# Kernel optimization log

Hardware: AMD Instinct MI355X
Metric: run time of the kernel (lower is better)

The kernel has to match this reference:

```python
import jax, jax.numpy as jnp
import numpy as np

B, P, Q, D_IN, H, DR = 16, 4096, 512, 512, 256, 256


def setup_inputs() -> dict:
    key = jax.random.key(0)
    ks = jax.random.split(key, 6)
    passage = jax.random.normal(ks[0], (B, P, D_IN), dtype=jnp.float32)
    question = jax.random.normal(ks[1], (B, Q, D_IN), dtype=jnp.float32)
    rep = jax.random.normal(ks[2], (B, Q, DR), dtype=jnp.float32)
    rep_p = jax.random.normal(ks[3], (B, P, DR), dtype=jnp.float32)
    p_mask = jnp.zeros((B, P), dtype=bool)  # True = padding position
    q_mask = jnp.zeros((B, Q), dtype=bool)
    # xavier-uniform-like init for U weight, stored as [in, out]
    limit = float(np.sqrt(6.0 / (D_IN + H)))
    W = jax.random.uniform(ks[4], (D_IN, H), dtype=jnp.float32, minval=-limit, maxval=limit)
    D = jnp.ones((1, H), dtype=jnp.float32)
    return {"passage": passage, "p_mask": p_mask, "question": question,
            "q_mask": q_mask, "rep": rep, "rep_p": rep_p, "W": W, "D": D,
            "is_training": 0}


def reference(passage, p_mask, question, q_mask, rep, rep_p, W, D, is_training):
    # inference path (is_training falsy): no dropout
    Up = jax.nn.relu(passage @ W)              # [B, P, H]
    Uq = jax.nn.relu(question @ W) * D         # [B, Q, H], scaled by diagonal D
    scores = jnp.einsum('bph,bqh->bpq', Up, Uq)  # [B, P, Q]
    # question -> passage direction (rep_p is not None)
    scores_T = jnp.where(p_mask[:, None, :], -jnp.inf, scores.transpose(0, 2, 1))  # [B, Q, P]
    alpha_p = jax.nn.softmax(scores_T, axis=-1)
    output_q = jnp.einsum('bqp,bpd->bqd', alpha_p, rep_p)  # [B, Q, DR]
    # passage -> question direction
    scores_m = jnp.where(q_mask[:, None, :], -jnp.inf, scores)  # [B, P, Q]
    alpha = jax.nn.softmax(scores_m, axis=-1)
    output = jnp.einsum('bpq,bqd->bpd', alpha, rep)  # [B, P, DR]
    return (output, output_q)
```

## Files before the change

### kernel.cpp

```cpp
#include <hip/hip_runtime.h>


typedef float  f32x4   __attribute__((ext_vector_type(4)));
typedef float  float4v __attribute__((ext_vector_type(4)));
typedef short  short8v __attribute__((ext_vector_type(8)));
typedef unsigned short us4 __attribute__((ext_vector_type(4)));
typedef unsigned short us8v __attribute__((ext_vector_type(8)));

#define MFMA16(a,b,c) __builtin_amdgcn_mfma_f32_16x16x32_bf16((a),(b),(c),0,0,0)

__device__ __forceinline__ unsigned short f2bf(float f) {
  unsigned int u = __builtin_bit_cast(unsigned int, f);
  u += 0x7FFFu + ((u >> 16) & 1u);
  return (unsigned short)(u >> 16);
}
__device__ __forceinline__ float bf2f(unsigned short h) {
  unsigned int u = (unsigned int)h << 16;
  return __builtin_bit_cast(float, u);
}
__device__ __forceinline__ void split2(float v, unsigned short& h, unsigned short& l) {
  h = f2bf(v);
  l = f2bf(v - bf2f(h));
}
__device__ __forceinline__ unsigned short enc16(float a, float cm) {
  float x = (a - cm + 20.f) * 3276.8f + 0.5f;
  x = fminf(fmaxf(x, 0.f), 65535.f);
  return (unsigned short)x;
}

__global__ __launch_bounds__(256) void transpose_all(
    const float* __restrict__ W, const float* __restrict__ rep,
    const float* __restrict__ rep_p,
    unsigned short* __restrict__ Wth, unsigned short* __restrict__ Wtl,
    unsigned short* __restrict__ repT, unsigned short* __restrict__ repTp)
{
  __shared__ float lTf[64][65];
  const int blk = blockIdx.x;
  const float* src; unsigned short* dst; unsigned short* dstl = nullptr;
  int srows; size_t r0, c0;
  if (blk < 4096) {
    int b = blk >> 8, tb = blk & 255;
    src = rep_p + (size_t)b * 4096 * 256;
    dst = repTp + (size_t)b * 256 * 4096;
    srows = 4096; r0 = (size_t)(tb >> 2) * 64; c0 = (size_t)(tb & 3) * 64;
  } else if (blk < 4608) {
    int rel = blk - 4096; int b = rel >> 5, tb = rel & 31;
    src = rep + (size_t)b * 512 * 256;
    dst = repT + (size_t)b * 256 * 512;
    srows = 512; r0 = (size_t)(tb >> 2) * 64; c0 = (size_t)(tb & 3) * 64;
  } else {
    int rel = blk - 4608;
    src = W; dst = Wth; dstl = Wtl;
    srows = 512; r0 = (size_t)(rel >> 2) * 64; c0 = (size_t)(rel & 3) * 64;
  }
  const int t = threadIdx.x;
#pragma unroll
  for (int j = 0; j < 4; ++j) {
    int idx = j * 256 + t;
    int r = idx >> 4, c4 = (idx & 15) * 4;
    float4v v = *(const float4v*)&src[(r0 + (size_t)r) * 256 + c0 + c4];
    lTf[r][c4 + 0] = v[0]; lTf[r][c4 + 1] = v[1];
    lTf[r][c4 + 2] = v[2]; lTf[r][c4 + 3] = v[3];
  }
  __syncthreads();
#pragma unroll
  for (int j = 0; j < 4; ++j) {
    int idx = j * 256 + t;
    int dr = idx >> 4, p4 = (idx & 15) * 4;
    size_t o = (c0 + (size_t)dr) * (size_t)srows + r0 + p4;
    if (!dstl) {
      us4 oh;
#pragma unroll
      for (int e = 0; e < 4; ++e) oh[e] = f2bf(lTf[p4 + e][dr]);
      *(us4*)&dst[o] = oh;
    } else {
      us4 oh, ol;
#pragma unroll
      for (int e = 0; e < 4; ++e) {
        unsigned short h, l; split2(lTf[p4 + e][dr], h, l);
        oh[e] = h; ol[e] = l;
      }
      *(us4*)&dst[o] = oh;
      *(us4*)&dstl[o] = ol;
    }
  }
}

template<int APPLY_D>
__global__ __launch_bounds__(256) void ugemm_kernel(
    const float* __restrict__ X,
    const unsigned short* __restrict__ Wth, const unsigned short* __restrict__ Wtl,
    const float* __restrict__ Dv,
    unsigned short* __restrict__ Uh, unsigned short* __restrict__ Ul)
{
  __shared__ unsigned short lAh[64 * 40], lAl[64 * 40];
  __shared__ unsigned short lBh[256 * 40], lBl[256 * 40];
  const int t = threadIdx.x;
  const int w = t >> 6, l = t & 63;
  const int l15 = l & 15, lg = l >> 4, kr = lg * 8;
  const size_t m0 = (size_t)blockIdx.x * 64;
  const int arow = t >> 2, ac = (t & 3) * 8;
  const float* asrc = X + (m0 + arow) * 512 + ac;

  f32x4 acc[4][4] = {};
  float4v va0, va1;
  short8v vbh[4], vbl[4];

  va0 = *(const float4v*)(asrc);
  va1 = *(const float4v*)(asrc + 4);
#pragma unroll
  for (int j = 0; j < 4; ++j) {
    int idx = j * 256 + t;
    int row = idx >> 2, c = (idx & 3) * 8;
    size_t g = (size_t)row * 512 + c;
    vbh[j] = *(const short8v*)&Wth[g];
    vbl[j] = *(const short8v*)&Wtl[g];
  }

  for (int k0 = 0; k0 < 512; k0 += 32) {
    short8v ph, pl;
#pragma unroll
    for (int e = 0; e < 4; ++e) {
      unsigned short h, lo;
      split2(va0[e], h, lo); ph[e] = (short)h; pl[e] = (short)lo;
      split2(va1[e], h, lo); ph[4 + e] = (short)h; pl[4 + e] = (short)lo;
    }
    __syncthreads();
    *(short8v*)&lAh[arow * 40 + ac] = ph;
    *(short8v*)&lAl[arow * 40 + ac] = pl;
#pragma unroll
    for (int j = 0; j < 4; ++j) {
      int idx = j * 256 + t;
      int row = idx >> 2, c = (idx & 3) * 8;
      *(short8v*)&lBh[row * 40 + c] = vbh[j];
      *(short8v*)&lBl[row * 40 + c] = vbl[j];
    }
    __syncthreads();
    if (k0 < 480) {
      va0 = *(const float4v*)(asrc + k0 + 32);
      va1 = *(const float4v*)(asrc + k0 + 36);
#pragma unroll
      for (int j = 0; j < 4; ++j) {
        int idx = j * 256 + t;
        int row = idx >> 2, c = (idx & 3) * 8;
        size_t g = (size_t)row * 512 + k0 + 32 + c;
        vbh[j] = *(const short8v*)&Wth[g];
        vbl[j] = *(const short8v*)&Wtl[g];
      }
    }
    short8v ah[4], al[4];
#pragma unroll
    for (int mi = 0; mi < 4; ++mi) {
      ah[mi] = *(const short8v*)&lAh[(mi * 16 + l15) * 40 + kr];
      al[mi] = *(const short8v*)&lAl[(mi * 16 + l15) * 40 + kr];
    }
#pragma unroll
    for (int ni = 0; ni < 4; ++ni) {
      int rr = (w * 64 + ni * 16 + l15) * 40 + kr;
      short8v bh = *(const short8v*)&lBh[rr];
      short8v bl = *(const short8v*)&lBl[rr];
#pragma unroll
      for (int mi = 0; mi < 4; ++mi) {
        acc[mi][ni] = MFMA16(ah[mi], bh, acc[mi][ni]);
        acc[mi][ni] = MFMA16(ah[mi], bl, acc[mi][ni]);
        acc[mi][ni] = MFMA16(al[mi], bh, acc[mi][ni]);
      }
    }
  }
#pragma unroll
  for (int mi = 0; mi < 4; ++mi)
#pragma unroll
    for (int ni = 0; ni < 4; ++ni)
#pragma unroll
      for (int r = 0; r < 4; ++r) {
        size_t row = m0 + mi * 16 + lg * 4 + r;
        int col = w * 64 + ni * 16 + l15;
        float v = acc[mi][ni][r];
        v = v > 0.f ? v : 0.f;
        if (APPLY_D) v *= Dv[col];
        unsigned short h, lo; split2(v, h, lo);
        Uh[row * 256 + col] = h;
        Ul[row * 256 + col] = lo;
      }
}

template<int STORE_S>
__global__ __launch_bounds__(512, 4) void dir2_kernel(
    const unsigned short* __restrict__ Uph, const unsigned short* __restrict__ Upl,
    const unsigned short* __restrict__ Uqh, const unsigned short* __restrict__ Uql,
    const unsigned short* __restrict__ repT, const unsigned char* __restrict__ qmask,
    const unsigned char* __restrict__ pmask, unsigned short* __restrict__ St,
    float* __restrict__ colmaxP, float* __restrict__ out)
{
  __shared__ __align__(16) unsigned char smem[68608];
  unsigned short* probs = (unsigned short*)smem;
  float* smax = (float*)(smem + 66560);
  float* ssum = (float*)(smem + 67584);

  const int id = blockIdx.x;
  const int b  = (id & 7) | ((id >> 9) << 3);
  const int p0 = ((id >> 3) & 63) * 64;
  const int t = threadIdx.x;
  const int w = t >> 6, l = t & 63;
  const int wr = w >> 2, wc = w & 3;
  const int l15 = l & 15, lg = l >> 4, kr = lg * 8;
  const int srow = t >> 2, sc = (t & 3) * 8;

  const unsigned short* UqBh = Uqh + (size_t)b * 512 * 256;
  const unsigned short* UqBl = Uql + (size_t)b * 512 * 256;
  const size_t aoff = ((size_t)b * 4096 + p0 + wr * 32 + l15) * 256 + kr;
  const unsigned short* pAh0 = Uph + aoff;
  const unsigned short* pAh1 = pAh0 + 16 * 256;
  const unsigned short* pAl0 = Upl + aoff;
  const unsigned short* pAl1 = pAl0 + 16 * 256;

  auto lbh = [&](int buf) { return (unsigned short*)(smem + buf * 20480); };
  auto lbl = [&](int buf) { return (unsigned short*)(smem + buf * 20480 + 10240); };

  f32x4 acc[2][8] = {};
  short8v cah0, cah1, cal0, cal1;
  short8v nah0, nah1, nal0, nal1;
  short8v rh, rl;

  cah0 = *(const short8v*)&pAh0[0];
  cah1 = *(const short8v*)&pAh1[0];
  cal0 = *(const short8v*)&pAl0[0];
  cal1 = *(const short8v*)&pAl1[0];
  {
    size_t g = (size_t)srow * 256 + sc;
    rh = *(const short8v*)&UqBh[g];
    rl = *(const short8v*)&UqBl[g];
  }
  *(short8v*)&lbh(0)[srow * 40 + sc] = rh;
  *(short8v*)&lbl(0)[srow * 40 + sc] = rl;
  __syncthreads();

  for (int k0 = 0; k0 < 8; ++k0) {
#pragma unroll
    for (int qh = 0; qh < 4; ++qh) {
      const int cur = qh & 1;
      const bool last = (k0 == 7) && (qh == 3);
      if (!last) {
        int nk0 = (qh == 3) ? k0 + 1 : k0;
        int nqh = (qh == 3) ? 0 : qh + 1;
        size_t g = (size_t)(nqh * 128 + srow) * 256 + nk0 * 32 + sc;
        rh = *(const short8v*)&UqBh[g];
        rl = *(const short8v*)&UqBl[g];
      }
      if (qh == 3 && k0 < 7) {
        size_t ao = (size_t)(k0 + 1) * 32;
        nah0 = *(const short8v*)&pAh0[ao];
        nah1 = *(const short8v*)&pAh1[ao];
        nal0 = *(const short8v*)&pAl0[ao];
        nal1 = *(const short8v*)&pAl1[ao];
      }
      const unsigned short* bhp = lbh(cur);
      const unsigned short* blp = lbl(cur);
#pragma unroll
      for (int qi = 0; qi < 2; ++qi) {
        int rr = (wc * 32 + qi * 16 + l15) * 40 + kr;
        short8v bh = *(const short8v*)&bhp[rr];
        short8v bl = *(const short8v*)&blp[rr];
        int j = qh * 2 + qi;
        acc[0][j] = MFMA16(cah0, bh, acc[0][j]);
        acc[0][j] = MFMA16(cah0, bl, acc[0][j]);
        acc[0][j] = MFMA16(cal0, bh, acc[0][j]);
        acc[1][j] = MFMA16(cah1, bh, acc[1][j]);
        acc[1][j] = MFMA16(cah1, bl, acc[1][j]);
        acc[1][j] = MFMA16(cal1, bh, acc[1][j]);
      }
      if (!last) {
        *(short8v*)&lbh(cur ^ 1)[srow * 40 + sc] = rh;
        *(short8v*)&lbl(cur ^ 1)[srow * 40 + sc] = rl;
      }
      if (qh == 3 && k0 < 7) { cah0 = nah0; cah1 = nah1; cal0 = nal0; cal1 = nal1; }
      __syncthreads();
    }
  }
  if (STORE_S) {
    const unsigned char* pmk = pmask + (size_t)b * 4096 + p0 + wr * 32;
    unsigned int pmw0 = *(const unsigned int*)&pmk[lg * 4];
    unsigned int pmw1 = *(const unsigned int*)&pmk[16 + lg * 4];
#pragma unroll
    for (int j = 0; j < 8; ++j) {
      int qcol = ((j >> 1) << 7) + wc * 32 + ((j & 1) << 4) + l15;
      float a0[4], a1[4];
      float cm = -1e30f;
#pragma unroll
      for (int r = 0; r < 4; ++r) {
        a0[r] = ((pmw0 >> (8 * r)) & 0xFFu) ? -1e30f : acc[0][j][r];
        a1[r] = ((pmw1 >> (8 * r)) & 0xFFu) ? -1e30f : acc[1][j][r];
        cm = fmaxf(cm, fmaxf(a0[r], a1[r]));
      }
      cm = fmaxf(cm, __shfl_xor(cm, 16));
      cm = fmaxf(cm, __shfl_xor(cm, 32));
      us4 e0, e1;
#pragma unroll
      for (int r = 0; r < 4; ++r) {
        e0[r] = enc16(a0[r], cm);
        e1[r] = enc16(a1[r], cm);
      }
      size_t sb = ((size_t)b * 512 + qcol) * 4096 + p0 + wr * 32 + lg * 4;
      *(us4*)&St[sb]      = e0;
      *(us4*)&St[sb + 16] = e1;
      if (l < 16)
        colmaxP[((size_t)b * 128 + (p0 >> 5) + wr) * 512 + qcol] = cm;
    }
  }
  const unsigned char* qm = qmask + (size_t)b * 512;
#pragma unroll
  for (int j = 0; j < 8; ++j) {
    int qcol = ((j >> 1) << 7) + wc * 32 + ((j & 1) << 4) + l15;
    if (qm[qcol]) {
#pragma unroll
      for (int mi = 0; mi < 2; ++mi)
#pragma unroll
        for (int r = 0; r < 4; ++r) acc[mi][j][r] = -1e30f;
    }
  }
#pragma unroll
  for (int mi = 0; mi < 2; ++mi)
#pragma unroll
    for (int r = 0; r < 4; ++r) {
      float v = acc[mi][0][r];
#pragma unroll
      for (int j = 1; j < 8; ++j) v = fmaxf(v, acc[mi][j][r]);
      v = fmaxf(v, __shfl_xor(v, 1)); v = fmaxf(v, __shfl_xor(v, 2));
      v = fmaxf(v, __shfl_xor(v, 4)); v = fmaxf(v, __shfl_xor(v, 8));
      if (l15 == 0) smax[wc * 64 + wr * 32 + mi * 16 + lg * 4 + r] = v;
    }
  __syncthreads();
  float Mx[2][4];
#pragma unroll
  for (int mi = 0; mi < 2; ++mi)
#pragma unroll
    for (int r = 0; r < 4; ++r) {
      int row = wr * 32 + mi * 16 + lg * 4 + r;
      Mx[mi][r] = fmaxf(fmaxf(smax[row], smax[64 + row]),
                        fmaxf(smax[128 + row], smax[192 + row]));
    }
  float rs[2][4] = {};
#pragma unroll
  for (int mi = 0; mi < 2; ++mi)
#pragma unroll
    for (int j = 0; j < 8; ++j)
#pragma unroll
      for (int r = 0; r < 4; ++r) {
        float ev = __expf(acc[mi][j][r] - Mx[mi][r]);
        acc[mi][j][r] = ev;
        rs[mi][r] += ev;
      }
#pragma unroll
  for (int mi = 0; mi < 2; ++mi)
#pragma unroll
    for (int r = 0; r < 4; ++r) {
      float v = rs[mi][r];
      v += __shfl_xor(v, 1); v += __shfl_xor(v, 2);
      v += __shfl_xor(v, 4); v += __shfl_xor(v, 8);
      if (l15 == 0) ssum[wc * 64 + wr * 32 + mi * 16 + lg * 4 + r] = v;
    }
#pragma unroll
  for (int mi = 0; mi < 2; ++mi)
#pragma unroll
    for (int j = 0; j < 8; ++j) {
      int qcol = ((j >> 1) << 7) + wc * 32 + ((j & 1) << 4) + l15;
#pragma unroll
      for (int r = 0; r < 4; ++r)
        probs[(wr * 32 + mi * 16 + lg * 4 + r) * 520 + qcol] = f2bf(acc[mi][j][r]);
    }
  __syncthreads();
  const unsigned short* rT = repT + (size_t)b * 131072;
  float invv[4][4];
#pragma unroll
  for (int mi = 0; mi < 4; ++mi)
#pragma unroll
    for (int r = 0; r < 4; ++r) {
      int row = mi * 16 + lg * 4 + r;
      invv[mi][r] = 1.0f / (ssum[row] + ssum[64 + row] +
                            ssum[128 + row] + ssum[192 + row]);
    }
  f32x4 acc2[4][2] = {};
  const unsigned short* rTb = rT + (size_t)(w * 32 + l15) * 512 + kr;
  short8v cb0 = *(const short8v*)(rTb);
  short8v cb1 = *(const short8v*)(rTb + 16 * 512);
  for (int k0 = 0; k0 < 512; k0 += 32) {
    int kn = (k0 + 32) & 511;
    short8v nb0 = *(const short8v*)(rTb + kn);
    short8v nb1 = *(const short8v*)(rTb + 16 * 512 + kn);
    short8v a0 = *(const short8v*)&probs[(l15) * 520 + k0 + kr];
    short8v a1 = *(const short8v*)&probs[(16 + l15) * 520 + k0 + kr];
    short8v a2 = *(const short8v*)&probs[(32 + l15) * 520 + k0 + kr];
    short8v a3 = *(const short8v*)&probs[(48 + l15) * 520 + k0 + kr];
    acc2[0][0] = MFMA16(a0, cb0, acc2[0][0]);
    acc2[1][0] = MFMA16(a1, cb0, acc2[1][0]);
    acc2[2][0] = MFMA16(a2, cb0, acc2[2][0]);
    acc2[3][0] = MFMA16(a3, cb0, acc2[3][0]);
    acc2[0][1] = MFMA16(a0, cb1, acc2[0][1]);
    acc2[1][1] = MFMA16(a1, cb1, acc2[1][1]);
    acc2[2][1] = MFMA16(a2, cb1, acc2[2][1]);
    acc2[3][1] = MFMA16(a3, cb1, acc2[3][1]);
    cb0 = nb0; cb1 = nb1;
  }
#pragma unroll
  for (int mi = 0; mi < 4; ++mi)
#pragma unroll
    for (int di = 0; di < 2; ++di)
#pragma unroll
      for (int r = 0; r < 4; ++r) {
        int row = p0 + mi * 16 + lg * 4 + r;
        int col = w * 32 + di * 16 + l15;
        out[((size_t)b * 4096 + row) * 256 + col] = acc2[mi][di][r] * invv[mi][r];
      }
}

__global__ __launch_bounds__(256) void dir1_pv(
    const unsigned short* __restrict__ St, const float* __restrict__ colmaxP,
    const unsigned short* __restrict__ repTp,
    float* __restrict__ accP, float* __restrict__ mlP)
{
  __shared__ unsigned short lAe[2][32 * 72];
  const int id = blockIdx.x;
  const int xcd = id & 7, r0 = id >> 3;
  const int b = xcd * 2 + (r0 >> 6);
  const int rem = r0 & 63;
  const int qt = rem >> 2, ch = rem & 3;
  const int q0 = qt * 32, pbeg = ch * 1024;
  const int pi = (b * 16 + qt) * 4 + ch;
  const int NT = 16;

  const int t = threadIdx.x;
  const int w = t >> 6, l = t & 63;
  const int l15 = l & 15, lg = l >> 4, kr = lg * 8;
  const int srow = t >> 3, sp = (t & 7) * 8;

  const float* cmq = colmaxP + (size_t)b * 128 * 512 + q0 + srow;
  float mq_s;
  {
    const int part = t & 7;
    float m = -1e30f;
#pragma unroll
    for (int j = 0; j < 16; ++j)
      m = fmaxf(m, cmq[(size_t)(part + j * 8) * 512]);
    m = fmaxf(m, __shfl_xor(m, 1));
    m = fmaxf(m, __shfl_xor(m, 2));
    m = fmaxf(m, __shfl_xor(m, 4));
    mq_s = m;
  }
  const unsigned short* Sb = St + ((size_t)b * 512 + q0 + srow) * 4096;
  const unsigned short* vtb = repTp + ((size_t)b * 256 + w * 64 + l15) * 4096;
  float rsum = 0.f;
  f32x4 acc[2][4] = {};
  us8v u; float cmv;
  short8v bvA[2][4], bvB[2][4];

  auto STAGE_LOAD = [&](int tile) {
    int pelem = pbeg + tile * 64 + sp;
    u = *(const us8v*)(Sb + pelem);
    cmv = cmq[(size_t)(pelem >> 5) * 512];
  };
  auto STAGE_FINISH = [&](int buf) {
    float base = cmv - 20.f - mq_s;
    short8v pk;
#pragma unroll
    for (int e = 0; e < 8; ++e) {
      float ev = __expf((float)u[e] * (1.f / 3276.8f) + base);
      rsum += ev;
      pk[e] = (short)f2bf(ev);
    }
    *(short8v*)&lAe[buf][srow * 72 + sp] = pk;
  };
  auto BV_LOAD = [&](int tile, short8v (&bv)[2][4]) {
    int p0v = pbeg + tile * 64;
#pragma unroll
    for (int ks = 0; ks < 2; ++ks)
#pragma unroll
      for (int di = 0; di < 4; ++di)
        bv[ks][di] = *(const short8v*)&vtb[(size_t)(di * 16) * 4096 + p0v + ks * 32 + kr];
  };
  auto COMPUTE = [&](int buf, short8v (&bv)[2][4]) {
#pragma unroll
    for (int ks = 0; ks < 2; ++ks) {
      short8v pa0 = *(const short8v*)&lAe[buf][l15 * 72 + ks * 32 + kr];
      short8v pa1 = *(const short8v*)&lAe[buf][(16 + l15) * 72 + ks * 32 + kr];
#pragma unroll
      for (int di = 0; di < 4; ++di) {
        acc[0][di] = MFMA16(pa0, bv[ks][di], acc[0][di]);
        acc[1][di] = MFMA16(pa1, bv[ks][di], acc[1][di]);
      }
    }
  };

  STAGE_LOAD(0);
  BV_LOAD(0, bvA);
  STAGE_FINISH(0);
  STAGE_LOAD(1);
  __syncthreads();

#pragma unroll 1
  for (int tt = 0; tt < NT; tt += 2) {
    const bool has1 = (tt + 1 < NT), has2 = (tt + 2 < NT), has3 = (tt + 3 < NT);
    if (has1) BV_LOAD(tt + 1, bvB);
    COMPUTE(0, bvA);
    if (has1) STAGE_FINISH(1);
    if (has2) STAGE_LOAD(tt + 2);
    __syncthreads();
    if (has1) {
      if (has2) BV_LOAD(tt + 2, bvA);
      COMPUTE(1, bvB);
      if (has2) STAGE_FINISH(0);
      if (has3) STAGE_LOAD(tt + 3);
      __syncthreads();
    }
  }

  rsum += __shfl_xor(rsum, 1);
  rsum += __shfl_xor(rsum, 2);
  rsum += __shfl_xor(rsum, 4);
  if ((t & 7) == 0) mlP[(size_t)pi * 32 + srow] = rsum;

  float* ab = accP + (size_t)pi * 32 * 256;
#pragma unroll
  for (int mi = 0; mi < 2; ++mi)
#pragma unroll
    for (int di = 0; di < 4; ++di)
#pragma unroll
      for (int r = 0; r < 4; ++r) {
        int row = mi * 16 + lg * 4 + r;
        int col = w * 64 + di * 16 + l15;
        ab[(size_t)row * 256 + col] = acc[mi][di][r];
      }
}

__global__ __launch_bounds__(256) void merge4_kernel(
    const float* __restrict__ accP, const float* __restrict__ mlP,
    float* __restrict__ outq)
{
  const int g = blockIdx.x * 256 + threadIdx.x;
  const int row = g >> 6;
  const int d0 = (g & 63) * 4;
  const int b = row >> 9, q = row & 511;
  const int qt = q >> 5, ri = q & 31;
  const int pbase = (b * 16 + qt) * 4;
  float s = 0.f;
  float4v o = {0.f, 0.f, 0.f, 0.f};
#pragma unroll
  for (int c = 0; c < 4; ++c) {
    s += mlP[(size_t)(pbase + c) * 32 + ri];
    float4v a = *(const float4v*)&accP[((size_t)(pbase + c) * 32 + ri) * 256 + d0];
#pragma unroll
    for (int k = 0; k < 4; ++k) o[k] += a[k];
  }
  float inv = 1.0f / s;
#pragma unroll
  for (int k = 0; k < 4; ++k) o[k] *= inv;
  *(float4v*)&outq[(size_t)row * 256 + d0] = o;
}

__global__ __launch_bounds__(256) void dir1_partial(
    const unsigned short* __restrict__ Uph, const unsigned short* __restrict__ Upl,
    const unsigned short* __restrict__ Uqh, const unsigned short* __restrict__ Uql,
    const unsigned short* __restrict__ repTp, const unsigned char* __restrict__ pmask,
    float* __restrict__ accP, float* __restrict__ mlP)
{
  __shared__ __align__(16) unsigned char smem[39424];
  unsigned short* lAh = (unsigned short*)smem;
  unsigned short* lAl = (unsigned short*)(smem + 16896);
  unsigned short* lP  = (unsigned short*)(smem + 33792);
  float* smax = (float*)(smem + 38400);
  float* ssum = (float*)(smem + 38912);

  const int id  = blockIdx.x;
  const int xcd = id & 7, rr0 = id >> 3;
  const int b   = xcd * 2 + (rr0 >> 6);
  const int rem = rr0 & 63;
  const int qt  = rem >> 2, ch = rem & 3;
  const int q0  = qt * 32;
  const int pbeg = ch * 1024;
  const int pi  = (b * 16 + qt) * 4 + ch;

  const int t = threadIdx.x;
  const int w = t >> 6, l = t & 63;
  const int l15 = l & 15, lg = l >> 4, kr = lg * 8;

#pragma unroll
  for (int j = 0; j < 4; ++j) {
    int idx = j * 256 + t;
    int row = idx >> 5, c = (idx & 31) * 8;
    size_t g = ((size_t)b * 512 + q0 + row) * 256 + c;
    *(short8v*)&lAh[row * 264 + c] = *(const short8v*)&Uqh[g];
    *(short8v*)&lAl[row * 264 + c] = *(const short8v*)&Uql[g];
  }
  float m_r[2][4], l_r[2][4];
#pragma unroll
  for (int mi = 0; mi < 2; ++mi)
#pragma unroll
    for (int r = 0; r < 4; ++r) { m_r[mi][r] = -1e30f; l_r[mi][r] = 0.f; }
  f32x4 accO[2][4] = {};
  const size_t upoff = ((size_t)b * 4096 + w * 16 + l15) * 256;
  const unsigned short* upbh = Uph + upoff;
  const unsigned short* upbl = Upl + upoff;
  const unsigned short* vtb = repTp + (size_t)b * 1048576;
  const unsigned char* pm = pmask + (size_t)b * 4096;
  __syncthreads();

  for (int p0 = pbeg; p0 < pbeg + 1024; p0 += 64) {
    f32x4 s[2] = {};
#pragma unroll
    for (int k0 = 0; k0 < 256; k0 += 32) {
      short8v ah0 = *(const short8v*)&lAh[l15 * 264 + k0 + kr];
      short8v ah1 = *(const short8v*)&lAh[(16 + l15) * 264 + k0 + kr];
      short8v al0 = *(const short8v*)&lAl[l15 * 264 + k0 + kr];
      short8v al1 = *(const short8v*)&lAl[(16 + l15) * 264 + k0 + kr];
      short8v bvh = *(const short8v*)&upbh[(size_t)p0 * 256 + k0 + kr];
      short8v bvl = *(const short8v*)&upbl[(size_t)p0 * 256 + k0 + kr];
      s[0] = MFMA16(ah0, bvh, s[0]);
      s[0] = MFMA16(ah0, bvl, s[0]);
      s[0] = MFMA16(al0, bvh, s[0]);
      s[1] = MFMA16(ah1, bvh, s[1]);
      s[1] = MFMA16(ah1, bvl, s[1]);
      s[1] = MFMA16(al1, bvh, s[1]);
    }
    if (pm[p0 + w * 16 + l15]) {
#pragma unroll
      for (int mi = 0; mi < 2; ++mi)
#pragma unroll
        for (int r = 0; r < 4; ++r) s[mi][r] = -1e30f;
    }
#pragma unroll
    for (int mi = 0; mi < 2; ++mi)
#pragma unroll
      for (int r = 0; r < 4; ++r) {
        float v = s[mi][r];
        v = fmaxf(v, __shfl_xor(v, 1)); v = fmaxf(v, __shfl_xor(v, 2));
        v = fmaxf(v, __shfl_xor(v, 4)); v = fmaxf(v, __shfl_xor(v, 8));
        if (l15 == 0) smax[w * 32 + mi * 16 + lg * 4 + r] = v;
      }
    __syncthreads();
    float mnew[2][4], fsc[2][4], e[2][4];
#pragma unroll
    for (int mi = 0; mi < 2; ++mi)
#pragma unroll
      for (int r = 0; r < 4; ++r) {
        int row = mi * 16 + lg * 4 + r;
        float tm = fmaxf(fmaxf(smax[row], smax[32 + row]),
                         fmaxf(smax[64 + row], smax[96 + row]));
        float mn = fmaxf(m_r[mi][r], tm);
        mnew[mi][r] = mn;
        fsc[mi][r] = __expf(m_r[mi][r] - mn);
        e[mi][r] = __expf(s[mi][r] - mn);
      }
#pragma unroll
    for (int mi = 0; mi < 2; ++mi)
#pragma unroll
      for (int r = 0; r < 4; ++r) {
        float v = e[mi][r];
        v += __shfl_xor(v, 1); v += __shfl_xor(v, 2);
        v += __shfl_xor(v, 4); v += __shfl_xor(v, 8);
        if (l15 == 0) ssum[w * 32 + mi * 16 + lg * 4 + r] = v;
        lP[(mi * 16 + lg * 4 + r) * 72 + w * 16 + l15] = f2bf(e[mi][r]);
      }
    __syncthreads();
#pragma unroll
    for (int mi = 0; mi < 2; ++mi)
#pragma unroll
      for (int r = 0; r < 4; ++r) {
        int row = mi * 16 + lg * 4 + r;
        float ts = ssum[row] + ssum[32 + row] + ssum[64 + row] + ssum[96 + row];
        l_r[mi][r] = l_r[mi][r] * fsc[mi][r] + ts;
        m_r[mi][r] = mnew[mi][r];
      }
#pragma unroll
    for (int mi = 0; mi < 2; ++mi)
#pragma unroll
      for (int di = 0; di < 4; ++di)
#pragma unroll
        for (int r = 0; r < 4; ++r) accO[mi][di][r] *= fsc[mi][r];
#pragma unroll
    for (int ks = 0; ks < 64; ks += 32) {
      short8v pa0 = *(const short8v*)&lP[l15 * 72 + ks + kr];
      short8v pa1 = *(const short8v*)&lP[(16 + l15) * 72 + ks + kr];
#pragma unroll
      for (int di = 0; di < 4; ++di) {
        short8v bv = *(const short8v*)&vtb[(size_t)(w * 64 + di * 16 + l15) * 4096 + p0 + ks + kr];
        accO[0][di] = MFMA16(pa0, bv, accO[0][di]);
        accO[1][di] = MFMA16(pa1, bv, accO[1][di]);
      }
    }
  }
  float* ab = accP + (size_t)pi * 32 * 256;
#pragma unroll
  for (int mi = 0; mi < 2; ++mi)
#pragma unroll
    for (int di = 0; di < 4; ++di)
#pragma unroll
      for (int r = 0; r < 4; ++r) {
        int row = mi * 16 + lg * 4 + r;
        int col = w * 64 + di * 16 + l15;
        ab[(size_t)row * 256 + col] = accO[mi][di][r];
      }
  if (w == 0 && l15 == 0) {
#pragma unroll
    for (int mi = 0; mi < 2; ++mi)
#pragma unroll
      for (int r = 0; r < 4; ++r) {
        int row = mi * 16 + lg * 4 + r;
        mlP[((size_t)pi * 32 + row) * 2 + 0] = m_r[mi][r];
        mlP[((size_t)pi * 32 + row) * 2 + 1] = l_r[mi][r];
      }
  }
}

__global__ __launch_bounds__(256) void merge_kernel(
    const float* __restrict__ accP, const float* __restrict__ mlP,
    float* __restrict__ outq)
{
  const int g = blockIdx.x * 256 + threadIdx.x;
  const int row = g >> 6;
  const int d0 = (g & 63) * 4;
  const int b = row >> 9, q = row & 511;
  const int qt = q >> 5, ri = q & 31;
  const int pbase = (b * 16 + qt) * 4;
  float m[4], lv[4];
  float M = -1e30f;
#pragma unroll
  for (int c = 0; c < 4; ++c) {
    m[c]  = mlP[((size_t)(pbase + c) * 32 + ri) * 2 + 0];
    lv[c] = mlP[((size_t)(pbase + c) * 32 + ri) * 2 + 1];
    M = fmaxf(M, m[c]);
  }
  float s = 0.f;
  float4v o = {0.f, 0.f, 0.f, 0.f};
#pragma unroll
  for (int c = 0; c < 4; ++c) {
    float e = __expf(m[c] - M);
    s += e * lv[c];
    float4v a = *(const float4v*)&accP[((size_t)(pbase + c) * 32 + ri) * 256 + d0];
#pragma unroll
    for (int k = 0; k < 4; ++k) o[k] += e * a[k];
  }
  float inv = 1.0f / s;
#pragma unroll
  for (int k = 0; k < 4; ++k) o[k] *= inv;
  *(float4v*)&outq[(size_t)row * 256 + d0] = o;
}

extern "C" void kernel_launch(void* const* d_in, const int* in_sizes, int n_in,
                              void* d_out, int out_size, void* d_ws, size_t ws_size,
                              hipStream_t stream) {
  (void)in_sizes; (void)n_in; (void)out_size;
  const float* passage        = (const float*)d_in[0];
  const unsigned char* p_mask = (const unsigned char*)d_in[1];
  const float* question       = (const float*)d_in[2];
  const unsigned char* q_mask = (const unsigned char*)d_in[3];
  const float* rep            = (const float*)d_in[4];
  const float* rep_p          = (const float*)d_in[5];
  const float* W              = (const float*)d_in[6];
  const float* Dv             = (const float*)d_in[7];

  unsigned short* Wth   = (unsigned short*)d_ws;
  unsigned short* Wtl   = Wth   + 131072;
  unsigned short* repT  = Wtl   + 131072;
  unsigned short* repTp = repT  + 2097152;
  unsigned short* Uqh   = repTp + 16777216;
  unsigned short* Uql   = Uqh   + 2097152;
  unsigned short* Uph   = Uql   + 2097152;
  unsigned short* Upl   = Uph   + 16777216;
  unsigned short* StU = (unsigned short*)((char*)d_ws + 113770496ULL);
  float* colmaxP      = (float*)((char*)d_ws + 180879360ULL);
  const size_t NEEDED = 185073664ULL;

  float* out  = (float*)d_out;
  float* outq = out + (size_t)16 * 4096 * 256;

  transpose_all<<<4640, 256, 0, stream>>>(W, rep, rep_p, Wth, Wtl, repT, repTp);
  ugemm_kernel<0><<<1024, 256, 0, stream>>>(passage,  Wth, Wtl, nullptr, Uph, Upl);
  ugemm_kernel<1><<<128,  256, 0, stream>>>(question, Wth, Wtl, Dv,      Uqh, Uql);

  if (ws_size >= NEEDED) {
    float* accP4 = (float*)Uph;
    float* mlP4  = (float*)Uqh;
    dir2_kernel<1><<<1024, 512, 0, stream>>>(Uph, Upl, Uqh, Uql, repT,
                                             q_mask, p_mask, StU, colmaxP, out);
    dir1_pv<<<1024, 256, 0, stream>>>(StU, colmaxP, repTp, accP4, mlP4);
    merge4_kernel<<<2048, 256, 0, stream>>>(accP4, mlP4, outq);
  } else {
    float* accP = out;
    float* mlP  = (float*)Wth;
    dir1_partial<<<1024, 256, 0, stream>>>(Uph, Upl, Uqh, Uql, repTp, p_mask, accP, mlP);
    merge_kernel<<<2048, 256, 0, stream>>>(accP, mlP, outq);
    dir2_kernel<0><<<1024, 512, 0, stream>>>(Uph, Upl, Uqh, Uql, repT,
                                             q_mask, nullptr, nullptr, nullptr, out);
  }
}
```

Before: 335.6 us.

## Merge U GEMMs and rep transposes into one heterogeneous prep kernel

Splits the W transpose into its own small kernel, then fuses the passage/question U GEMMs and the rep/rep_p transposes into a single launch whose blocks dispatch on block index. The aim is to overlap the memory-bound transposes with the GEMM work and to remove launch gaps and tail effects between the separate prep kernels. In exchange, every block of the fused kernel reserves 51 KB of shared memory, including the transpose blocks, which may lower their occupancy. The fallback path keeps the original kernels.

```diff
diff --git a/kernel.cpp b/kernel.cpp
--- a/kernel.cpp
+++ b/kernel.cpp
@@ -28,39 +28,18 @@
   return (unsigned short)x;
 }
 
-__global__ __launch_bounds__(256) void transpose_all(
-    const float* __restrict__ W, const float* __restrict__ rep,
-    const float* __restrict__ rep_p,
-    unsigned short* __restrict__ Wth, unsigned short* __restrict__ Wtl,
-    unsigned short* __restrict__ repT, unsigned short* __restrict__ repTp)
-{
-  __shared__ float lTf[64][65];
-  const int blk = blockIdx.x;
-  const float* src; unsigned short* dst; unsigned short* dstl = nullptr;
-  int srows; size_t r0, c0;
-  if (blk < 4096) {
-    int b = blk >> 8, tb = blk & 255;
-    src = rep_p + (size_t)b * 4096 * 256;
-    dst = repTp + (size_t)b * 256 * 4096;
-    srows = 4096; r0 = (size_t)(tb >> 2) * 64; c0 = (size_t)(tb & 3) * 64;
-  } else if (blk < 4608) {
-    int rel = blk - 4096; int b = rel >> 5, tb = rel & 31;
-    src = rep + (size_t)b * 512 * 256;
-    dst = repT + (size_t)b * 256 * 512;
-    srows = 512; r0 = (size_t)(tb >> 2) * 64; c0 = (size_t)(tb & 3) * 64;
-  } else {
-    int rel = blk - 4608;
-    src = W; dst = Wth; dstl = Wtl;
-    srows = 512; r0 = (size_t)(rel >> 2) * 64; c0 = (size_t)(rel & 3) * 64;
-  }
-  const int t = threadIdx.x;
+__device__ __forceinline__ void transpose_body(
+    const float* __restrict__ src, unsigned short* __restrict__ dst,
+    unsigned short* __restrict__ dstl, int srows, size_t r0, size_t c0,
+    int t, float* smemf)
+{
 #pragma unroll
   for (int j = 0; j < 4; ++j) {
     int idx = j * 256 + t;
     int r = idx >> 4, c4 = (idx & 15) * 4;
     float4v v = *(const float4v*)&src[(r0 + (size_t)r) * 256 + c0 + c4];
-    lTf[r][c4 + 0] = v[0]; lTf[r][c4 + 1] = v[1];
-    lTf[r][c4 + 2] = v[2]; lTf[r][c4 + 3] = v[3];
+    smemf[r * 65 + c4 + 0] = v[0]; smemf[r * 65 + c4 + 1] = v[1];
+    smemf[r * 65 + c4 + 2] = v[2]; smemf[r * 65 + c4 + 3] = v[3];
   }
   __syncthreads();
 #pragma unroll
@@ -71,13 +50,13 @@
     if (!dstl) {
       us4 oh;
 #pragma unroll
-      for (int e = 0; e < 4; ++e) oh[e] = f2bf(lTf[p4 + e][dr]);
+      for (int e = 0; e < 4; ++e) oh[e] = f2bf(smemf[(p4 + e) * 65 + dr]);
       *(us4*)&dst[o] = oh;
     } else {
       us4 oh, ol;
 #pragma unroll
       for (int e = 0; e < 4; ++e) {
-        unsigned short h, l; split2(lTf[p4 + e][dr], h, l);
+        unsigned short h, l; split2(smemf[(p4 + e) * 65 + dr], h, l);
         oh[e] = h; ol[e] = l;
       }
       *(us4*)&dst[o] = oh;
@@ -87,18 +66,19 @@
 }
 
 template<int APPLY_D>
-__global__ __launch_bounds__(256) void ugemm_kernel(
+__device__ __forceinline__ void ugemm_body(
     const float* __restrict__ X,
     const unsigned short* __restrict__ Wth, const unsigned short* __restrict__ Wtl,
     const float* __restrict__ Dv,
-    unsigned short* __restrict__ Uh, unsigned short* __restrict__ Ul)
-{
-  __shared__ unsigned short lAh[64 * 40], lAl[64 * 40];
-  __shared__ unsigned short lBh[256 * 40], lBl[256 * 40];
-  const int t = threadIdx.x;
+    unsigned short* __restrict__ Uh, unsigned short* __restrict__ Ul,
+    size_t m0, int t, unsigned char* smem)
+{
+  unsigned short* lAh = (unsigned short*)smem;
+  unsigned short* lAl = (unsigned short*)(smem + 5120);
+  unsigned short* lBh = (unsigned short*)(smem + 10240);
+  unsigned short* lBl = (unsigned short*)(smem + 30720);
   const int w = t >> 6, l = t & 63;
   const int l15 = l & 15, lg = l >> 4, kr = lg * 8;
-  const size_t m0 = (size_t)blockIdx.x * 64;
   const int arow = t >> 2, ac = (t & 3) * 8;
   const float* asrc = X + (m0 + arow) * 512 + ac;
 
@@ -182,6 +162,89 @@
         Uh[row * 256 + col] = h;
         Ul[row * 256 + col] = lo;
       }
+}
+
+__global__ __launch_bounds__(256) void transpose_w(
+    const float* __restrict__ W,
+    unsigned short* __restrict__ Wth, unsigned short* __restrict__ Wtl)
+{
+  __shared__ float lTf[64 * 65];
+  const int blk = blockIdx.x;
+  transpose_body(W, Wth, Wtl, 512, (size_t)(blk >> 2) * 64,
+                 (size_t)(blk & 3) * 64, threadIdx.x, lTf);
+}
+
+__global__ __launch_bounds__(256) void prep_mega(
+    const float* __restrict__ passage, const float* __restrict__ question,
+    const float* __restrict__ rep, const float* __restrict__ rep_p,
+    const unsigned short* __restrict__ Wth, const unsigned short* __restrict__ Wtl,
+    const float* __restrict__ Dv,
+    unsigned short* __restrict__ Uph, unsigned short* __restrict__ Upl,
+    unsigned short* __restrict__ Uqh, unsigned short* __restrict__ Uql,
+    unsigned short* __restrict__ repT, unsigned short* __restrict__ repTp)
+{
+  __shared__ __align__(16) unsigned char smem[51200];
+  const int blk = blockIdx.x;
+  const int t = threadIdx.x;
+  if (blk < 1024) {
+    ugemm_body<0>(passage, Wth, Wtl, nullptr, Uph, Upl,
+                  (size_t)blk * 64, t, smem);
+  } else if (blk < 1152) {
+    ugemm_body<1>(question, Wth, Wtl, Dv, Uqh, Uql,
+                  (size_t)(blk - 1024) * 64, t, smem);
+  } else if (blk < 5248) {
+    int rel = blk - 1152;
+    int b = rel >> 8, tb = rel & 255;
+    transpose_body(rep_p + (size_t)b * 4096 * 256,
+                   repTp + (size_t)b * 256 * 4096, nullptr, 4096,
+                   (size_t)(tb >> 2) * 64, (size_t)(tb & 3) * 64, t,
+                   (float*)smem);
+  } else {
+    int rel = blk - 5248;
+    int b = rel >> 5, tb = rel & 31;
+    transpose_body(rep + (size_t)b * 512 * 256,
+                   repT + (size_t)b * 256 * 512, nullptr, 512,
+                   (size_t)(tb >> 2) * 64, (size_t)(tb & 3) * 64, t,
+                   (float*)smem);
+  }
+}
+
+__global__ __launch_bounds__(256) void transpose_all(
+    const float* __restrict__ W, const float* __restrict__ rep,
+    const float* __restrict__ rep_p,
+    unsigned short* __restrict__ Wth, unsigned short* __restrict__ Wtl,
+    unsigned short* __restrict__ repT, unsigned short* __restrict__ repTp)
+{
+  __shared__ float lTf[64 * 65];
+  const int blk = blockIdx.x;
+  const int t = threadIdx.x;
+  if (blk < 4096) {
+    int b = blk >> 8, tb = blk & 255;
+    transpose_body(rep_p + (size_t)b * 4096 * 256,
+                   repTp + (size_t)b * 256 * 4096, nullptr, 4096,
+                   (size_t)(tb >> 2) * 64, (size_t)(tb & 3) * 64, t, lTf);
+  } else if (blk < 4608) {
+    int rel = blk - 4096; int b = rel >> 5, tb = rel & 31;
+    transpose_body(rep + (size_t)b * 512 * 256,
+                   repT + (size_t)b * 256 * 512, nullptr, 512,
+                   (size_t)(tb >> 2) * 64, (size_t)(tb & 3) * 64, t, lTf);
+  } else {
+    int rel = blk - 4608;
+    transpose_body(W, Wth, Wtl, 512, (size_t)(rel >> 2) * 64,
+                   (size_t)(rel & 3) * 64, t, lTf);
+  }
+}
+
+template<int APPLY_D>
+__global__ __launch_bounds__(256) void ugemm_kernel(
+    const float* __restrict__ X,
+    const unsigned short* __restrict__ Wth, const unsigned short* __restrict__ Wtl,
+    const float* __restrict__ Dv,
+    unsigned short* __restrict__ Uh, unsigned short* __restrict__ Ul)
+{
+  __shared__ __align__(16) unsigned char smem[51200];
+  ugemm_body<APPLY_D>(X, Wth, Wtl, Dv, Uh, Ul,
+                      (size_t)blockIdx.x * 64, threadIdx.x, smem);
 }
 
 template<int STORE_S>
@@ -772,13 +835,13 @@
   float* out  = (float*)d_out;
   float* outq = out + (size_t)16 * 4096 * 256;
 
-  transpose_all<<<4640, 256, 0, stream>>>(W, rep, rep_p, Wth, Wtl, repT, repTp);
-  ugemm_kernel<0><<<1024, 256, 0, stream>>>(passage,  Wth, Wtl, nullptr, Uph, Upl);
-  ugemm_kernel<1><<<128,  256, 0, stream>>>(question, Wth, Wtl, Dv,      Uqh, Uql);
-
   if (ws_size >= NEEDED) {
     float* accP4 = (float*)Uph;
     float* mlP4  = (float*)Uqh;
+    transpose_w<<<32, 256, 0, stream>>>(W, Wth, Wtl);
+    prep_mega<<<5760, 256, 0, stream>>>(passage, question, rep, rep_p,
+                                        Wth, Wtl, Dv, Uph, Upl, Uqh, Uql,
+                                        repT, repTp);
     dir2_kernel<1><<<1024, 512, 0, stream>>>(Uph, Upl, Uqh, Uql, repT,
                                              q_mask, p_mask, StU, colmaxP, out);
     dir1_pv<<<1024, 256, 0, stream>>>(StU, colmaxP, repTp, accP4, mlP4);
@@ -786,6 +849,9 @@
   } else {
     float* accP = out;
     float* mlP  = (float*)Wth;
+    transpose_all<<<4640, 256, 0, stream>>>(W, rep, rep_p, Wth, Wtl, repT, repTp);
+    ugemm_kernel<0><<<1024, 256, 0, stream>>>(passage,  Wth, Wtl, nullptr, Uph, Upl);
+    ugemm_kernel<1><<<128,  256, 0, stream>>>(question, Wth, Wtl, Dv,      Uqh, Uql);
     dir1_partial<<<1024, 256, 0, stream>>>(Uph, Upl, Uqh, Uql, repTp, p_mask, accP, mlP);
     merge_kernel<<<2048, 256, 0, stream>>>(accP, mlP, outq);
     dir2_kernel<0><<<1024, 512, 0, stream>>>(Uph, Upl, Uqh, Uql, repT,
```

Result: faster. 312.2 us (-7.0%).
